# Kernel tuning notes

Measured on AMD Instinct MI355X. Metric: run time of the kernel, lower is better.

Reference implementation:

```python
import jax, jax.numpy as jnp
import numpy as np

ALPHA = 0.2  # LeakyReLU negative slope
NEG_INF = -9e15


def setup_inputs() -> dict:
    key = jax.random.key(0)
    k1, k2, k3, k4 = jax.random.split(key, 4)
    B, N, F_in, F_out = 8, 2048, 256, 128
    h = jax.random.normal(k1, (B, N, F_in), dtype=jnp.float32)
    adj = jax.random.randint(k2, (B, N, N), 0, 2, dtype=jnp.int32)
    # xavier_uniform with gain=1.414
    def xavier(k, shape, gain=1.414):
        fan_in, fan_out = shape[0], shape[1]
        limit = gain * np.sqrt(6.0 / (fan_in + fan_out))
        return jax.random.uniform(k, shape, jnp.float32, -limit, limit)
    W = xavier(k3, (F_in, F_out))
    a = xavier(k4, (2 * F_out, 1))
    return {"h": h, "adj": adj, "W": W, "a": a}


def reference(h, adj, W, a):
    # h: [B,N,F_in], adj: [B,N,N], W: [F_in,F_out], a: [2*F_out,1]
    Wh = jnp.einsum('bnf,fe->bne', h, W)  # [B,N,E]
    E = Wh.shape[-1]
    a_src, a_dst = a[:E, 0], a[E:, 0]
    # e[b,i,j] = leakyrelu(Wh[b,i].a_src + Wh[b,j].a_dst)  (additive decomposition
    # of a @ concat(Wh_i, Wh_j) -- same math, no [B,N,N,2E] intermediate)
    s_src = Wh @ a_src  # [B,N]
    s_dst = Wh @ a_dst  # [B,N]
    e = jax.nn.leaky_relu(s_src[:, :, None] + s_dst[:, None, :], negative_slope=ALPHA)
    e = jnp.where(adj > 0, e, NEG_INF)
    attention = jax.nn.softmax(e, axis=2)  # [B,N,N]
    # dropout p=0.0 / eval mode -> identity
    h_prime = jnp.einsum('bij,bje->bie', attention, Wh)
    return jax.nn.elu(h_prime)  # concat=True
```

## Files before the change

### kernel.cpp

```cpp
#include <hip/hip_runtime.h>
#include <hip/hip_bf16.h>

#define GAT_ALPHA 0.2f
#define LOG2E 1.4426950408889634f

typedef float f32x4 __attribute__((ext_vector_type(4)));
typedef int   i32x4 __attribute__((ext_vector_type(4)));
typedef short bf16x8 __attribute__((ext_vector_type(8)));

static constexpr int Nn  = 2048;
static constexpr int FIN = 256;
static constexpr int FO  = 128;

static __device__ __forceinline__ unsigned short f2bf(float x) {
    __hip_bfloat16 h = __float2bfloat16(x);
    return __builtin_bit_cast(unsigned short, h);
}
static __device__ __forceinline__ float bf2f(unsigned short u) {
    unsigned int v = ((unsigned int)u) << 16;
    return __builtin_bit_cast(float, v);
}

__global__ __launch_bounds__(256) void gat_prep(
        const float* __restrict__ W, const float* __restrict__ a,
        float* __restrict__ wa, unsigned int* __restrict__ md_key)
{
    __shared__ float pr[32][8];
    __shared__ float pd[32][8];
    const int t = threadIdx.x;
    const int kl = t >> 3, seg = t & 7;
    const int k = blockIdx.x * 32 + kl;
    float ps = 0.f, pv = 0.f;
    const float* wr = W + (size_t)k * FO + seg * 16;
    #pragma unroll
    for (int f = 0; f < 16; f += 4) {
        f32x4 wv = *(const f32x4*)(wr + f);
        f32x4 as = *(const f32x4*)(a + seg * 16 + f);
        f32x4 ad = *(const f32x4*)(a + FO + seg * 16 + f);
        ps += wv[0]*as[0] + wv[1]*as[1] + wv[2]*as[2] + wv[3]*as[3];
        pv += wv[0]*ad[0] + wv[1]*ad[1] + wv[2]*ad[2] + wv[3]*ad[3];
    }
    pr[kl][seg] = ps; pd[kl][seg] = pv;
    __syncthreads();
    if (t < 32) {
        float s = 0.f, d = 0.f;
        #pragma unroll
        for (int j = 0; j < 8; ++j) { s += pr[t][j]; d += pd[t][j]; }
        wa[blockIdx.x * 32 + t]       = s;
        wa[256 + blockIdx.x * 32 + t] = d;
    }
    if (blockIdx.x == 0 && t < 8) md_key[t] = 0u;
}

__global__ __launch_bounds__(256) void gat_wh(
        const float* __restrict__ h, const float* __restrict__ W,
        const float* __restrict__ wa, unsigned short* __restrict__ WhT,
        float* __restrict__ s_src, float* __restrict__ s_dst,
        unsigned int* __restrict__ md_key)
{
    __shared__ unsigned short WT[FO][264];
    __shared__ float wal[512];
    __shared__ float sred[64][4][2];
    __shared__ float red64[64];
    const int t  = threadIdx.x;
    const int b  = blockIdx.x & 7;
    const int n0 = (blockIdx.x >> 3) << 6;

    if (t < 128) *(f32x4*)&wal[t * 4] = *(const f32x4*)&wa[t * 4];
    #pragma unroll
    for (int c = 0; c < 32; ++c) {
        int flat = c * 1024 + t * 4;
        int k = flat >> 7, f = flat & 127;
        f32x4 wv = *(const f32x4*)&W[flat];
        WT[f + 0][k] = f2bf(wv[0]);
        WT[f + 1][k] = f2bf(wv[1]);
        WT[f + 2][k] = f2bf(wv[2]);
        WT[f + 3][k] = f2bf(wv[3]);
    }
    __syncthreads();

    {
        const int row = t >> 2, seg = t & 3;
        const float* hp  = h + ((size_t)(b * Nn + n0 + row)) * FIN + seg * 64;
        const float* was = &wal[seg * 64];
        const float* wad = &wal[256 + seg * 64];
        float ps = 0.f, pv = 0.f;
        #pragma unroll
        for (int j = 0; j < 64; j += 4) {
            f32x4 hv = *(const f32x4*)(hp + j);
            f32x4 sv = *(const f32x4*)(was + j);
            f32x4 dv = *(const f32x4*)(wad + j);
            ps += hv[0]*sv[0] + hv[1]*sv[1] + hv[2]*sv[2] + hv[3]*sv[3];
            pv += hv[0]*dv[0] + hv[1]*dv[1] + hv[2]*dv[2] + hv[3]*dv[3];
        }
        sred[row][seg][0] = ps;
        sred[row][seg][1] = pv;
    }
    __syncthreads();
    if (t < 64) {
        float s = sred[t][0][0] + sred[t][1][0] + sred[t][2][0] + sred[t][3][0];
        float d = sred[t][0][1] + sred[t][1][1] + sred[t][2][1] + sred[t][3][1];
        s_src[b * Nn + n0 + t] = s;
        s_dst[b * Nn + n0 + t] = d;
        red64[t] = d;
    }
    __syncthreads();
    if (t < 16) red64[t] = fmaxf(fmaxf(red64[t], red64[t + 16]),
                                 fmaxf(red64[t + 32], red64[t + 48]));
    __syncthreads();
    if (t == 0) {
        float m = red64[0];
        #pragma unroll
        for (int j = 1; j < 16; ++j) m = fmaxf(m, red64[j]);
        unsigned int bits = __builtin_bit_cast(unsigned int, m);
        unsigned int key  = (bits & 0x80000000u) ? ~bits : (bits | 0x80000000u);
        atomicMax(md_key + b, key);
    }

    const int w = t >> 6, lane = t & 63, n16 = lane & 15, quad = lane >> 4;
    const float* ha = h + ((size_t)(b * Nn + n0 + w * 16 + n16)) * FIN + quad * 8;
    f32x4 acc[8] = {};
    #pragma unroll
    for (int ks = 0; ks < 8; ++ks) {
        f32x4 h0 = *(const f32x4*)(ha + ks * 32);
        f32x4 h1 = *(const f32x4*)(ha + ks * 32 + 4);
        bf16x8 af;
        af[0] = (short)f2bf(h0[0]); af[1] = (short)f2bf(h0[1]);
        af[2] = (short)f2bf(h0[2]); af[3] = (short)f2bf(h0[3]);
        af[4] = (short)f2bf(h1[0]); af[5] = (short)f2bf(h1[1]);
        af[6] = (short)f2bf(h1[2]); af[7] = (short)f2bf(h1[3]);
        #pragma unroll
        for (int nt = 0; nt < 8; ++nt) {
            bf16x8 bfr = *(const bf16x8*)&WT[nt * 16 + n16][ks * 32 + quad * 8];
            acc[nt] = __builtin_amdgcn_mfma_f32_16x16x32_bf16(af, bfr, acc[nt], 0, 0, 0);
        }
    }
    #pragma unroll
    for (int nt = 0; nt < 8; ++nt) {
        ushort4 pk;
        pk.x = f2bf(acc[nt][0]); pk.y = f2bf(acc[nt][1]);
        pk.z = f2bf(acc[nt][2]); pk.w = f2bf(acc[nt][3]);
        *(ushort4*)&WhT[((size_t)(b * FO + nt * 16 + n16)) * Nn + n0 + w * 16 + quad * 4] = pk;
    }
}

__global__ __launch_bounds__(256, 4) void gat_attn(
        const int* __restrict__ adj, const unsigned short* __restrict__ WhT,
        const float* __restrict__ s_src, const float* __restrict__ s_dst,
        const unsigned int* __restrict__ md_key, float* __restrict__ out)
{
    __shared__ float accbuf[2][16][FO];
    __shared__ float l_red[16];
    const int t = threadIdx.x, w = t >> 6, lane = t & 63;
    const int n16 = lane & 15, quad = lane >> 4;
    const int b  = blockIdx.x & 7;
    const int i0 = (blockIdx.x >> 3) << 4;

    const unsigned int key = md_key[b];
    const unsigned int mb  = (key & 0x80000000u) ? (key ^ 0x80000000u) : ~key;
    const float mdb = __builtin_bit_cast(float, mb);
    const float ss  = s_src[b * Nn + i0 + n16];
    const float tm  = ss + mdb;
    const float mi  = fmaxf(tm, GAT_ALPHA * tm) * LOG2E;
    const float ssL = ss * LOG2E;

    const int* aptr = adj + ((size_t)(b * Nn + i0 + n16)) * Nn + quad * 8;
    const float* dptr = s_dst + b * Nn + quad * 8;
    const unsigned short* wptr = WhT + ((size_t)(b * FO + n16)) * Nn + quad * 8;

    f32x4 acc[8] = {};
    float ls = 0.f;
    int jc = w * 32;
    i32x4 A0 = *(const i32x4*)(aptr + jc), A1 = *(const i32x4*)(aptr + jc + 4);
    f32x4 D0 = *(const f32x4*)(dptr + jc), D1 = *(const f32x4*)(dptr + jc + 4);

    for (int s = 0; s < 16; ++s) {
        const int jp = (s < 15) ? (jc + 128) : (w * 32);
        i32x4 nA0 = *(const i32x4*)(aptr + jp);
        i32x4 nA1 = *(const i32x4*)(aptr + jp + 4);
        f32x4 nD0 = *(const f32x4*)(dptr + jp);
        f32x4 nD1 = *(const f32x4*)(dptr + jp + 4);

        float dv[8] = {D0[0],D0[1],D0[2],D0[3],D1[0],D1[1],D1[2],D1[3]};
        int   am[8] = {A0[0],A0[1],A0[2],A0[3],A1[0],A1[1],A1[2],A1[3]};
        bf16x8 af;
        #pragma unroll
        for (int j = 0; j < 8; ++j) {
            float u  = __builtin_fmaf(dv[j], LOG2E, ssL);
            float lr = fmaxf(u, GAT_ALPHA * u);
            float e  = __builtin_amdgcn_exp2f(lr - mi);
            e = (am[j] > 0) ? e : 0.f;
            unsigned short ub = f2bf(e);
            af[j] = (short)ub;
            ls += bf2f(ub);
        }
        #pragma unroll
        for (int nt = 0; nt < 8; ++nt) {
            bf16x8 bfr = *(const bf16x8*)(wptr + (size_t)(nt * 16) * Nn + jc);
            acc[nt] = __builtin_amdgcn_mfma_f32_16x16x32_bf16(af, bfr, acc[nt], 0, 0, 0);
        }
        jc = jc + 128; A0 = nA0; A1 = nA1; D0 = nD0; D1 = nD1;
    }

    if (t < 16) l_red[t] = 0.f;
    __syncthreads();
    atomicAdd(&l_red[n16], ls);
    if (w < 2) {
        #pragma unroll
        for (int nt = 0; nt < 8; ++nt)
            #pragma unroll
            for (int r = 0; r < 4; ++r)
                accbuf[w][quad * 4 + r][nt * 16 + n16] = acc[nt][r];
    }
    __syncthreads();
    if (w >= 2) {
        #pragma unroll
        for (int nt = 0; nt < 8; ++nt)
            #pragma unroll
            for (int r = 0; r < 4; ++r)
                accbuf[w - 2][quad * 4 + r][nt * 16 + n16] += acc[nt][r];
    }
    __syncthreads();
    float* ob = out + ((size_t)(b * Nn + i0)) * FO;
    #pragma unroll
    for (int r = 0; r < 2; ++r) {
        int flat = (r << 10) + (t << 2);
        int m = flat >> 7;
        int f = flat & 127;
        f32x4 v0 = *(const f32x4*)&accbuf[0][m][f];
        f32x4 v1 = *(const f32x4*)&accbuf[1][m][f];
        float l = l_red[m];
        f32x4 o;
        #pragma unroll
        for (int j = 0; j < 4; ++j) {
            float x = (v0[j] + v1[j]) / l;
            o[j] = x > 0.f ? x : expm1f(x);
        }
        *(f32x4*)&ob[(size_t)m * FO + f] = o;
    }
}

extern "C" void kernel_launch(void* const* d_in, const int* in_sizes, int n_in,
                              void* d_out, int out_size, void* d_ws, size_t ws_size,
                              hipStream_t stream)
{
    const float* h   = (const float*)d_in[0];
    const int*   adj = (const int*)d_in[1];
    const float* W   = (const float*)d_in[2];
    const float* a   = (const float*)d_in[3];
    float* out = (float*)d_out;

    char* ws = (char*)d_ws;
    unsigned short* WhT = (unsigned short*)ws;
    float* s_src        = (float*)(ws + 4194304);
    float* s_dst        = (float*)(ws + 4259840);
    float* wa           = (float*)(ws + 4325376);
    unsigned int* md_key= (unsigned int*)(ws + 4327424);

    hipLaunchKernelGGL(gat_prep, dim3(8),    dim3(256), 0, stream, W, a, wa, md_key);
    hipLaunchKernelGGL(gat_wh,   dim3(256),  dim3(256), 0, stream, h, W, wa, WhT, s_src, s_dst, md_key);
    hipLaunchKernelGGL(gat_attn, dim3(1024), dim3(256), 0, stream, adj, WhT, s_src, s_dst, md_key, out);
}
```

Baseline: 275.7 us.

## Process 32 rows per block and stage Wh tiles and probabilities in LDS

Doubles the row tile of the attention kernel to 32 rows per block, halving the grid, so each loaded WhT chunk is reused across twice as many query rows. WhT chunks and the bf16 attention probabilities are written to shared memory and reloaded as MFMA fragments. Adjacency loads are restructured so each thread reads contiguous pieces of one row. This costs two block barriers per iteration, more LDS, and a lower occupancy bound of 3 blocks.

Measured after the change: 234.5 us. -15.0%, faster.

```diff
diff --git a/kernel.cpp b/kernel.cpp
--- a/kernel.cpp
+++ b/kernel.cpp
@@ -144,91 +144,124 @@
     }
 }
 
-__global__ __launch_bounds__(256, 4) void gat_attn(
+__global__ __launch_bounds__(256, 3) void gat_attn(
         const int* __restrict__ adj, const unsigned short* __restrict__ WhT,
         const float* __restrict__ s_src, const float* __restrict__ s_dst,
         const unsigned int* __restrict__ md_key, float* __restrict__ out)
 {
-    __shared__ float accbuf[2][16][FO];
-    __shared__ float l_red[16];
+    constexpr int WS = 136;
+    constexpr int PS = 136;
+    constexpr int AS = 132;
+    __shared__ __align__(16) unsigned short whs[128 * WS];
+    __shared__ __align__(16) unsigned short psT[32 * PS];
+    __shared__ float l_red[32];
+    float* accbuf = (float*)whs;
+
     const int t = threadIdx.x, w = t >> 6, lane = t & 63;
     const int n16 = lane & 15, quad = lane >> 4;
     const int b  = blockIdx.x & 7;
-    const int i0 = (blockIdx.x >> 3) << 4;
+    const int i0 = (blockIdx.x >> 3) << 5;
+    const int r  = t >> 3;
+    const int jg = t & 7;
+
+    if (t < 32) l_red[t] = 0.f;
 
     const unsigned int key = md_key[b];
     const unsigned int mb  = (key & 0x80000000u) ? (key ^ 0x80000000u) : ~key;
     const float mdb = __builtin_bit_cast(float, mb);
-    const float ss  = s_src[b * Nn + i0 + n16];
-    const float tm  = ss + mdb;
+    const float ssr = s_src[b * Nn + i0 + r];
+    const float tm  = ssr + mdb;
     const float mi  = fmaxf(tm, GAT_ALPHA * tm) * LOG2E;
-    const float ssL = ss * LOG2E;
-
-    const int* aptr = adj + ((size_t)(b * Nn + i0 + n16)) * Nn + quad * 8;
-    const float* dptr = s_dst + b * Nn + quad * 8;
-    const unsigned short* wptr = WhT + ((size_t)(b * FO + n16)) * Nn + quad * 8;
-
-    f32x4 acc[8] = {};
+    const float ssL = ssr * LOG2E;
+
+    const int* arow = adj + ((size_t)(b * Nn + i0 + r)) * Nn;
+    const float* dB = s_dst + b * Nn;
+    const unsigned short* wrow = WhT + ((size_t)(b * FO + (w << 5))) * Nn;
+    const int fsub = lane >> 4;
+    const int jc16 = lane & 15;
+
+    f32x4 acc[2][8] = {};
     float ls = 0.f;
-    int jc = w * 32;
-    i32x4 A0 = *(const i32x4*)(aptr + jc), A1 = *(const i32x4*)(aptr + jc + 4);
-    f32x4 D0 = *(const f32x4*)(dptr + jc), D1 = *(const f32x4*)(dptr + jc + 4);
+
+    i32x4 pa[4];
+    #pragma unroll
+    for (int k = 0; k < 4; ++k) pa[k] = *(const i32x4*)(arow + (jg << 2) + (k << 5));
 
     for (int s = 0; s < 16; ++s) {
-        const int jp = (s < 15) ? (jc + 128) : (w * 32);
-        i32x4 nA0 = *(const i32x4*)(aptr + jp);
-        i32x4 nA1 = *(const i32x4*)(aptr + jp + 4);
-        f32x4 nD0 = *(const f32x4*)(dptr + jp);
-        f32x4 nD1 = *(const f32x4*)(dptr + jp + 4);
-
-        float dv[8] = {D0[0],D0[1],D0[2],D0[3],D1[0],D1[1],D1[2],D1[3]};
-        int   am[8] = {A0[0],A0[1],A0[2],A0[3],A1[0],A1[1],A1[2],A1[3]};
-        bf16x8 af;
-        #pragma unroll
-        for (int j = 0; j < 8; ++j) {
-            float u  = __builtin_fmaf(dv[j], LOG2E, ssL);
-            float lr = fmaxf(u, GAT_ALPHA * u);
-            float e  = __builtin_amdgcn_exp2f(lr - mi);
-            e = (am[j] > 0) ? e : 0.f;
-            unsigned short ub = f2bf(e);
-            af[j] = (short)ub;
-            ls += bf2f(ub);
-        }
-        #pragma unroll
-        for (int nt = 0; nt < 8; ++nt) {
-            bf16x8 bfr = *(const bf16x8*)(wptr + (size_t)(nt * 16) * Nn + jc);
-            acc[nt] = __builtin_amdgcn_mfma_f32_16x16x32_bf16(af, bfr, acc[nt], 0, 0, 0);
-        }
-        jc = jc + 128; A0 = nA0; A1 = nA1; D0 = nD0; D1 = nD1;
-    }
-
-    if (t < 16) l_red[t] = 0.f;
-    __syncthreads();
-    atomicAdd(&l_red[n16], ls);
+        const int j0 = s << 7;
+        bf16x8 wreg[8];
+        #pragma unroll
+        for (int i = 0; i < 8; ++i)
+            wreg[i] = *(const bf16x8*)(wrow + (size_t)((i << 2) + fsub) * Nn + j0 + (jc16 << 3));
+        float e16[16];
+        #pragma unroll
+        for (int k = 0; k < 4; ++k) {
+            f32x4 dv = *(const f32x4*)(dB + j0 + (jg << 2) + (k << 5));
+            #pragma unroll
+            for (int j = 0; j < 4; ++j) {
+                float u  = __builtin_fmaf(dv[j], LOG2E, ssL);
+                float lr = fmaxf(u, GAT_ALPHA * u);
+                float e  = __builtin_amdgcn_exp2f(lr - mi);
+                e16[k * 4 + j] = (pa[k][j] > 0) ? e : 0.f;
+            }
+        }
+        const int jn = (s < 15) ? (j0 + 128) : 0;
+        #pragma unroll
+        for (int k = 0; k < 4; ++k) pa[k] = *(const i32x4*)(arow + jn + (jg << 2) + (k << 5));
+        #pragma unroll
+        for (int k = 0; k < 4; ++k) {
+            unsigned short u0 = f2bf(e16[k*4+0]), u1 = f2bf(e16[k*4+1]);
+            unsigned short u2 = f2bf(e16[k*4+2]), u3 = f2bf(e16[k*4+3]);
+            ls += bf2f(u0) + bf2f(u1) + bf2f(u2) + bf2f(u3);
+            ushort4 pk; pk.x = u0; pk.y = u1; pk.z = u2; pk.w = u3;
+            *(ushort4*)&psT[r * PS + (jg << 2) + (k << 5)] = pk;
+        }
+        #pragma unroll
+        for (int i = 0; i < 8; ++i)
+            *(bf16x8*)&whs[((w << 5) + (i << 2) + fsub) * WS + (jc16 << 3)] = wreg[i];
+        __syncthreads();
+        bf16x8 bfr[8];
+        #pragma unroll
+        for (int nt = 0; nt < 8; ++nt)
+            bfr[nt] = *(const bf16x8*)&whs[((nt << 4) + n16) * WS + (w << 5) + (quad << 3)];
+        #pragma unroll
+        for (int ig = 0; ig < 2; ++ig) {
+            bf16x8 af = *(const bf16x8*)&psT[((ig << 4) + n16) * PS + (w << 5) + (quad << 3)];
+            #pragma unroll
+            for (int nt = 0; nt < 8; ++nt)
+                acc[ig][nt] = __builtin_amdgcn_mfma_f32_16x16x32_bf16(af, bfr[nt], acc[ig][nt], 0, 0, 0);
+        }
+        __syncthreads();
+    }
+
+    atomicAdd(&l_red[r], ls);
     if (w < 2) {
         #pragma unroll
-        for (int nt = 0; nt < 8; ++nt)
-            #pragma unroll
-            for (int r = 0; r < 4; ++r)
-                accbuf[w][quad * 4 + r][nt * 16 + n16] = acc[nt][r];
+        for (int ig = 0; ig < 2; ++ig)
+            #pragma unroll
+            for (int nt = 0; nt < 8; ++nt)
+                #pragma unroll
+                for (int rr = 0; rr < 4; ++rr)
+                    accbuf[(size_t)w * 32 * AS + (ig * 16 + quad * 4 + rr) * AS + nt * 16 + n16] = acc[ig][nt][rr];
     }
     __syncthreads();
     if (w >= 2) {
         #pragma unroll
-        for (int nt = 0; nt < 8; ++nt)
-            #pragma unroll
-            for (int r = 0; r < 4; ++r)
-                accbuf[w - 2][quad * 4 + r][nt * 16 + n16] += acc[nt][r];
+        for (int ig = 0; ig < 2; ++ig)
+            #pragma unroll
+            for (int nt = 0; nt < 8; ++nt)
+                #pragma unroll
+                for (int rr = 0; rr < 4; ++rr)
+                    accbuf[(size_t)(w - 2) * 32 * AS + (ig * 16 + quad * 4 + rr) * AS + nt * 16 + n16] += acc[ig][nt][rr];
     }
     __syncthreads();
     float* ob = out + ((size_t)(b * Nn + i0)) * FO;
     #pragma unroll
-    for (int r = 0; r < 2; ++r) {
-        int flat = (r << 10) + (t << 2);
-        int m = flat >> 7;
-        int f = flat & 127;
-        f32x4 v0 = *(const f32x4*)&accbuf[0][m][f];
-        f32x4 v1 = *(const f32x4*)&accbuf[1][m][f];
+    for (int c = 0; c < 4; ++c) {
+        int flat = c * 1024 + t * 4;
+        int m = flat >> 7, f = flat & 127;
+        f32x4 v0 = *(const f32x4*)&accbuf[(size_t)m * AS + f];
+        f32x4 v1 = *(const f32x4*)&accbuf[(size_t)32 * AS + m * AS + f];
         float l = l_red[m];
         f32x4 o;
         #pragma unroll
@@ -257,7 +290,7 @@
     float* wa           = (float*)(ws + 4325376);
     unsigned int* md_key= (unsigned int*)(ws + 4327424);
 
-    hipLaunchKernelGGL(gat_prep, dim3(8),    dim3(256), 0, stream, W, a, wa, md_key);
-    hipLaunchKernelGGL(gat_wh,   dim3(256),  dim3(256), 0, stream, h, W, wa, WhT, s_src, s_dst, md_key);
-    hipLaunchKernelGGL(gat_attn, dim3(1024), dim3(256), 0, stream, adj, WhT, s_src, s_dst, md_key, out);
-}
+    hipLaunchKernelGGL(gat_prep, dim3(8),   dim3(256), 0, stream, W, a, wa, md_key);
+    hipLaunchKernelGGL(gat_wh,   dim3(256), dim3(256), 0, stream, h, W, wa, WhT, s_src, s_dst, md_key);
+    hipLaunchKernelGGL(gat_attn, dim3(512), dim3(256), 0, stream, adj, WhT, s_src, s_dst, md_key, out);
+}
```
